# Kernel optimization log

Measured on AMD Instinct MI355X. Metric: run time of the kernel, lower is better.

Reference implementation:

```python
import jax, jax.numpy as jnp
import numpy as np
import math

BL, N, T, C, H = 16, 256, 32, 256, 4
HD = C // H
GEOM_DIM = 12
K_REL = 32
LN_EPS = 1e-5
GEPS = 1e-6
NEG = -1e9


def setup_inputs() -> dict:
    key = jax.random.key(0)
    ks = jax.random.split(key, 24)
    s = 0.02  # weight init scale
    d = {
        "x": jax.random.normal(ks[0], (BL, N, C), jnp.float32),
        "lang_fea": jax.random.normal(ks[1], (BL, T, C), jnp.float32),
        "centers": jax.random.normal(ks[2], (BL, N, 3), jnp.float32),
        "corners": jax.random.normal(ks[3], (BL, N, 8, 3), jnp.float32),
        "obj_mask": jnp.ones((BL, N), dtype=bool),
        # LayerNorm
        "ln_g": jnp.ones((C,), jnp.float32),
        "ln_b": jnp.zeros((C,), jnp.float32),
        # qkv / proj
        "W_qkv": s * jax.random.normal(ks[4], (C, 3 * C), jnp.float32),
        "b_qkv": jnp.zeros((3 * C,), jnp.float32),
        "W_proj": s * jax.random.normal(ks[5], (C, C), jnp.float32),
        "b_proj": jnp.zeros((C,), jnp.float32),
        # geom2bias MLP (12 -> C -> H)
        "Wg1": s * jax.random.normal(ks[6], (GEOM_DIM, C), jnp.float32),
        "bg1": jnp.zeros((C,), jnp.float32),
        "Wg2": s * jax.random.normal(ks[7], (C, H), jnp.float32),
        "bg2": jnp.zeros((H,), jnp.float32),
        # txt2head MLP (C -> C -> H)
        "Wt1": s * jax.random.normal(ks[8], (C, C), jnp.float32),
        "bt1": jnp.zeros((C,), jnp.float32),
        "Wt2": s * jax.random.normal(ks[9], (C, H), jnp.float32),
        "bt2": jnp.zeros((H,), jnp.float32),
        "alpha": jnp.float32(0.05),
    }
    return d


def _build_relation_geom(centers, corners):
    # centers: (BL,N,3), corners: (BL,N,8,3) -> (BL,N,N,12)
    rel_vec = centers[:, None, :, :] - centers[:, :, None, :]  # (BL,N,N,3) j - i
    dist = jnp.linalg.norm(rel_vec, axis=-1, keepdims=True)
    horiz_dist = jnp.linalg.norm(rel_vec[..., :2], axis=-1, keepdims=True)
    delta_z = rel_vec[..., 2:3]
    cos_elev = delta_z / (dist + GEPS)
    sizes = corners.max(axis=2) - corners.min(axis=2)  # (BL,N,3)
    size_i = sizes[:, :, None, :]
    size_j = sizes[:, None, :, :]
    size_diff = size_j - size_i
    size_ratio = size_j / (size_i + GEPS)
    return jnp.concatenate([rel_vec, dist, horiz_dist, cos_elev, size_diff, size_ratio], axis=-1)


def _knn_mask(centers, k):
    # (BL,N,N) bool: each row i keeps its k nearest columns j (incl. self)
    diff = centers[:, :, None, :] - centers[:, None, :, :]
    dist = jnp.linalg.norm(diff, axis=-1)  # (BL,N,N)
    _, idx = jax.lax.top_k(-dist, k)  # smallest-k indices, (BL,N,k)
    return jnp.any(jax.nn.one_hot(idx, dist.shape[-1], dtype=bool), axis=-2)


def reference(x, lang_fea, centers, corners, obj_mask, ln_g, ln_b,
              W_qkv, b_qkv, W_proj, b_proj, Wg1, bg1, Wg2, bg2,
              Wt1, bt1, Wt2, bt2, alpha):
    # geometric pairwise bias: (BL,N,N,12) -> MLP -> (BL,H,N,N)
    geom = _build_relation_geom(centers, corners)
    bias = jax.nn.gelu(geom @ Wg1 + bg1, approximate=False) @ Wg2 + bg2
    bias = jnp.transpose(bias, (0, 3, 1, 2))  # (BL,H,N,N)

    # language-conditioned head gate: (BL,H,1,1)
    sent = lang_fea.mean(axis=1)  # (BL,C)
    head_w = jax.nn.sigmoid(jax.nn.gelu(sent @ Wt1 + bt1, approximate=False) @ Wt2 + bt2)
    head_w = head_w[:, :, None, None]

    warm = 1.0  # epoch=None -> no warmup scaling

    knn_mask = _knn_mask(centers, K_REL)
    pair = obj_mask[:, :, None] & obj_mask[:, None, :]
    attn_mask = knn_mask & pair  # (BL,N,N)

    residual = x
    # LayerNorm
    mu = x.mean(axis=-1, keepdims=True)
    var = x.var(axis=-1, keepdims=True)
    xn = (x - mu) * jax.lax.rsqrt(var + LN_EPS) * ln_g + ln_b

    qkv = (xn @ W_qkv + b_qkv).reshape(BL, N, 3, H, HD)
    q = jnp.transpose(qkv[:, :, 0], (0, 2, 1, 3))  # (BL,H,N,HD)
    k = jnp.transpose(qkv[:, :, 1], (0, 2, 1, 3))
    v = jnp.transpose(qkv[:, :, 2], (0, 2, 1, 3))

    logits = jnp.einsum("bhid,bhjd->bhij", q, k) / math.sqrt(HD)
    bias_eff = warm * alpha * head_w * bias
    logits = logits + bias_eff
    logits = jnp.where(attn_mask[:, None, :, :], logits, NEG)

    attn = jax.nn.softmax(logits, axis=-1)  # dropout is identity at eval
    out = jnp.einsum("bhij,bhjd->bhid", attn, v)
    out = jnp.transpose(out, (0, 2, 1, 3)).reshape(BL, N, C)
    out = out @ W_proj + b_proj
    x_out = residual + out
    return (x_out, jax.lax.stop_gradient(attn), jax.lax.stop_gradient(bias_eff))
```

## Files before the change

### kernel.cpp

```cpp
#include <hip/hip_runtime.h>
#include <math.h>

#define BLn 16
#define Nn 256
#define Tn 32
#define Cn 256
#define Hn 4
#define HDn 64
#define KREL 32

typedef float f32x4 __attribute__((ext_vector_type(4)));
typedef __bf16 bf16x8 __attribute__((ext_vector_type(8)));
typedef _Float16 f16x4 __attribute__((ext_vector_type(4)));
typedef _Float16 f16x2 __attribute__((ext_vector_type(2)));

#define MFMA16(a, b, c) __builtin_amdgcn_mfma_f32_16x16x32_bf16(a, b, c, 0, 0, 0)
#define MFMA16H(a, b, c) __builtin_amdgcn_mfma_f32_16x16x16f16(a, b, c, 0, 0, 0)

__device__ __forceinline__ float gelu_exact(float x) {
    return 0.5f * x * (1.0f + erff(x * 0.70710678118654752440f));
}

__device__ __forceinline__ f16x2 gelu_pk(f16x2 x) {
    const f16x2 P4 = {(_Float16)4.0f, (_Float16)4.0f};
    const f16x2 M4 = {(_Float16)-4.0f, (_Float16)-4.0f};
    const f16x2 C0 = {(_Float16)0.833076f, (_Float16)0.833076f};
    const f16x2 C1 = {(_Float16)-0.139388f, (_Float16)-0.139388f};
    const f16x2 C2 = {(_Float16)0.013040f, (_Float16)0.013040f};
    const f16x2 C3 = {(_Float16)-0.000413f, (_Float16)-0.000413f};
    const f16x2 HF = {(_Float16)0.5f, (_Float16)0.5f};
    f16x2 xc = __builtin_elementwise_min(__builtin_elementwise_max(x, M4), P4);
    f16x2 v = xc * xc;
    f16x2 w = C3 * v + C2;
    w = w * v + C1;
    w = w * v + C0;
    f16x2 t = w * xc;
    f16x2 s = t * HF + HF;
    return x * s;
}

__global__ void __launch_bounds__(256) k_prep(
    const float* __restrict__ x, const float* __restrict__ ln_g, const float* __restrict__ ln_b,
    __bf16* __restrict__ xnb, const float* __restrict__ centers, const int* __restrict__ obj,
    unsigned char* __restrict__ knn, const float* __restrict__ corners,
    float* __restrict__ sizes, const float* __restrict__ lang, const float* __restrict__ Wt1,
    const float* __restrict__ bt1, const float* __restrict__ Wt2, const float* __restrict__ bt2,
    float* __restrict__ headw, const float* __restrict__ W_qkv, __bf16* __restrict__ wqT,
    const float* __restrict__ W_proj, __bf16* __restrict__ wpT) {
    __shared__ float4 d4[64];
    __shared__ float sm1[Nn];
    __shared__ float ss[4], qq[4];
    __shared__ float T[64][65];
    float* sm0 = (float*)d4;
    int blk = blockIdx.x;
    int tid = threadIdx.x;

    if (blk < 4096) {
        int row = blk;
        int c = tid;
        float v = x[(size_t)row * Cn + c];
        float s = v, q = v * v;
        for (int m = 32; m > 0; m >>= 1) {
            s += __shfl_xor(s, m, 64);
            q += __shfl_xor(q, m, 64);
        }
        int w = c >> 6, l = c & 63;
        if (l == 0) { ss[w] = s; qq[w] = q; }
        __syncthreads();
        s = ss[0] + ss[1] + ss[2] + ss[3];
        q = qq[0] + qq[1] + qq[2] + qq[3];
        float mu = s * (1.0f / Cn);
        float var = q * (1.0f / Cn) - mu * mu;
        float r = rsqrtf(var + 1e-5f);
        xnb[(size_t)row * Cn + c] = (__bf16)((v - mu) * r * ln_g[c] + ln_b[c]);
    } else if (blk < 8192) {
        int bi = blk - 4096;
        int b = bi >> 8, i = bi & 255;
        int j = tid;
        float cx = centers[(b * Nn + i) * 3 + 0];
        float cy = centers[(b * Nn + i) * 3 + 1];
        float cz = centers[(b * Nn + i) * 3 + 2];
        float dx = centers[(b * Nn + j) * 3 + 0] - cx;
        float dy = centers[(b * Nn + j) * 3 + 1] - cy;
        float dz = centers[(b * Nn + j) * 3 + 2] - cz;
        float dd = sqrtf(dx * dx + dy * dy + dz * dz);
        sm0[j] = dd;
        __syncthreads();
        int rank = 0;
        for (int t4 = 0; t4 < 64; t4++) {
            float4 o = d4[t4];
            int t = t4 * 4;
            rank += (o.x < dd) || (o.x == dd && t + 0 < j);
            rank += (o.y < dd) || (o.y == dd && t + 1 < j);
            rank += (o.z < dd) || (o.z == dd && t + 2 < j);
            rank += (o.w < dd) || (o.w == dd && t + 3 < j);
        }
        bool m = (rank < KREL);
        m = m && (obj[b * Nn + i] != 0) && (obj[b * Nn + j] != 0);
        knn[(size_t)bi * Nn + j] = m ? 1 : 0;
    } else if (blk < 8208) {
        int b = blk - 8192, n = tid;
        const float* p = corners + (size_t)((b * Nn + n) * 8) * 3;
        float mn[3] = {1e30f, 1e30f, 1e30f}, mx[3] = {-1e30f, -1e30f, -1e30f};
        for (int v = 0; v < 8; v++)
            for (int d = 0; d < 3; d++) {
                float t = p[v * 3 + d];
                mn[d] = fminf(mn[d], t);
                mx[d] = fmaxf(mx[d], t);
            }
        for (int d = 0; d < 3; d++) sizes[(b * Nn + n) * 3 + d] = mx[d] - mn[d];
    } else if (blk < 8224) {
        int b = blk - 8208, c = tid;
        float s = 0.0f;
        for (int t = 0; t < Tn; t++) s += lang[((size_t)b * Tn + t) * Cn + c];
        sm0[c] = s * (1.0f / Tn);
        __syncthreads();
        float acc = bt1[c];
        for (int i = 0; i < Cn; i++) acc += sm0[i] * Wt1[i * Cn + c];
        sm1[c] = gelu_exact(acc);
        __syncthreads();
        if (c < Hn) {
            float a = bt2[c];
            for (int i = 0; i < Cn; i++) a += sm1[i] * Wt2[i * Hn + c];
            headw[b * Hn + c] = 1.0f / (1.0f + expf(-a));
        }
    } else if (blk < 8272) {
        int t = blk - 8224;
        int kt = t & 3, ot = t >> 2;
        for (int itr = 0; itr < 16; itr++) {
            int idx = itr * 256 + tid;
            int r = idx >> 6, c = idx & 63;
            T[r][c] = W_qkv[(size_t)(kt * 64 + r) * 768 + ot * 64 + c];
        }
        __syncthreads();
        for (int itr = 0; itr < 16; itr++) {
            int idx = itr * 256 + tid;
            int r = idx >> 6, c = idx & 63;
            wqT[(size_t)(ot * 64 + r) * 256 + kt * 64 + c] = (__bf16)T[c][r];
        }
    } else {
        int t = blk - 8272;
        int kt = t & 3, ot = t >> 2;
        for (int itr = 0; itr < 16; itr++) {
            int idx = itr * 256 + tid;
            int r = idx >> 6, c = idx & 63;
            T[r][c] = W_proj[(size_t)(kt * 64 + r) * 256 + ot * 64 + c];
        }
        __syncthreads();
        for (int itr = 0; itr < 16; itr++) {
            int idx = itr * 256 + tid;
            int r = idx >> 6, c = idx & 63;
            wpT[(size_t)(ot * 64 + r) * 256 + kt * 64 + c] = (__bf16)T[c][r];
        }
    }
}

__global__ void __launch_bounds__(256, 7) k_heavy(
    const float* __restrict__ centers, const float* __restrict__ sizes,
    const float* __restrict__ Wg1, const float* __restrict__ bg1,
    const float* __restrict__ Wg2, const float* __restrict__ bg2,
    const float* __restrict__ headw, const float* __restrict__ alphap,
    float* __restrict__ bias_eff, const __bf16* __restrict__ xnb,
    const __bf16* __restrict__ wqT, const float* __restrict__ bqkv,
    __bf16* __restrict__ qkvb) {
    __shared__ __align__(16) _Float16 fT[Nn][20];
    __shared__ __align__(16) _Float16 W1T[Cn][20];
    __shared__ __align__(16) _Float16 W2T[4][264];

    int blk = blockIdx.x;
    int tid = threadIdx.x;

    if (blk >= 4096) {
        int t = blk - 4096;
        int ib = t & 63, y = t >> 6;
        int w = tid >> 6, l = tid & 63, lr = l & 15, lg = l >> 4;
        const __bf16* arow = xnb + (size_t)(ib * 64 + w * 16 + lr) * Cn;

        f32x4 acc[4];
#pragma unroll
        for (int ot = 0; ot < 4; ot++) acc[ot] = (f32x4){0.f, 0.f, 0.f, 0.f};
#pragma unroll
        for (int kc = 0; kc < 8; kc++) {
            bf16x8 af = *(const bf16x8*)(arow + kc * 32 + lg * 8);
#pragma unroll
            for (int ot = 0; ot < 4; ot++) {
                bf16x8 bfr = *(const bf16x8*)(wqT + (size_t)(y * 64 + ot * 16 + lr) * Cn +
                                              kc * 32 + lg * 8);
                acc[ot] = MFMA16(af, bfr, acc[ot]);
            }
        }
        int seg = y >> 2, h = y & 3;
        __bf16* segp = qkvb + (size_t)seg * 1048576;
#pragma unroll
        for (int ot = 0; ot < 4; ot++) {
            float bo = bqkv[y * 64 + ot * 16 + lr];
#pragma unroll
            for (int r = 0; r < 4; r++) {
                int ig = ib * 64 + w * 16 + lg * 4 + r;
                int b = ig >> 8, n = ig & 255;
                segp[(((size_t)(b * Hn + h)) * Nn + n) * HDn + ot * 16 + lr] =
                    (__bf16)(acc[ot][r] + bo);
            }
        }
        return;
    }

    int b = blk >> 8, i = blk & 255;

    {
        int c = tid;
        _Float16 t1[20];
#pragma unroll
        for (int k = 0; k < 12; k++) t1[k] = (_Float16)Wg1[k * Cn + c];
        t1[12] = (_Float16)bg1[c];
#pragma unroll
        for (int k = 13; k < 20; k++) t1[k] = (_Float16)0.f;
#pragma unroll
        for (int q = 0; q < 5; q++) *(uint2*)&W1T[c][q * 4] = *(uint2*)&t1[q * 4];
#pragma unroll
        for (int h = 0; h < Hn; h++) W2T[h][c] = (_Float16)Wg2[c * Hn + h];
    }
    {
        int j = tid;
        float ci0 = centers[(b * Nn + i) * 3 + 0];
        float ci1 = centers[(b * Nn + i) * 3 + 1];
        float ci2 = centers[(b * Nn + i) * 3 + 2];
        float si0 = sizes[(b * Nn + i) * 3 + 0];
        float si1 = sizes[(b * Nn + i) * 3 + 1];
        float si2 = sizes[(b * Nn + i) * 3 + 2];
        float cj0 = centers[(b * Nn + j) * 3 + 0];
        float cj1 = centers[(b * Nn + j) * 3 + 1];
        float cj2 = centers[(b * Nn + j) * 3 + 2];
        float sj0 = sizes[(b * Nn + j) * 3 + 0];
        float sj1 = sizes[(b * Nn + j) * 3 + 1];
        float sj2 = sizes[(b * Nn + j) * 3 + 2];
        float rx = cj0 - ci0, ry = cj1 - ci1, rz = cj2 - ci2;
        float h2 = rx * rx + ry * ry;
        float dist = sqrtf(h2 + rz * rz);
        float horiz = sqrtf(h2);
        float f[16];
        f[0] = rx; f[1] = ry; f[2] = rz;
        f[3] = dist; f[4] = horiz;
        f[5] = rz / (dist + 1e-6f);
        f[6] = sj0 - si0; f[7] = sj1 - si1; f[8] = sj2 - si2;
        f[9] = sj0 / (si0 + 1e-6f);
        f[10] = sj1 / (si1 + 1e-6f);
        f[11] = sj2 / (si2 + 1e-6f);
        f[12] = 1.0f;
        _Float16 tf[20];
#pragma unroll
        for (int k = 0; k < 13; k++) tf[k] = (_Float16)f[k];
#pragma unroll
        for (int k = 13; k < 20; k++) tf[k] = (_Float16)0.f;
#pragma unroll
        for (int q = 0; q < 5; q++) *(uint2*)&fT[j][q * 4] = *(uint2*)&tf[q * 4];
    }
    __syncthreads();

    int w = tid >> 6, l = tid & 63;
    int lr = l & 15, lg = l >> 4;
    int jw = w * 64;
    int lrc = (lr < Hn) ? lr : 3;
    bool hr = (lr < Hn);

    f32x4 zero4 = {0.f, 0.f, 0.f, 0.f};
    f16x4 zf4 = {(_Float16)0.f, (_Float16)0.f, (_Float16)0.f, (_Float16)0.f};

    f16x4 bf_[4];
#pragma unroll
    for (int jt = 0; jt < 4; jt++) bf_[jt] = *(const f16x4*)&fT[jw + jt * 16 + lr][lg * 4];

    f32x4 pacc[4];
#pragma unroll
    for (int jt = 0; jt < 4; jt++) pacc[jt] = zero4;

#pragma unroll 2
    for (int cw = 0; cw < 16; cw++) {
        int cbase = cw * 16;
        f16x4 aw = *(const f16x4*)&W1T[cbase + lr][lg * 4];
        f16x4 w2v = *(const f16x4*)&W2T[lrc][cbase + lg * 4];
        f16x4 b2 = hr ? w2v : zf4;
#pragma unroll
        for (int jt = 0; jt < 4; jt++) {
            f32x4 acc = MFMA16H(aw, bf_[jt], zero4);
            f16x2 h01 = __builtin_bit_cast(f16x2, __builtin_amdgcn_cvt_pkrtz(acc[0], acc[1]));
            f16x2 h23 = __builtin_bit_cast(f16x2, __builtin_amdgcn_cvt_pkrtz(acc[2], acc[3]));
            h01 = gelu_pk(h01);
            h23 = gelu_pk(h23);
            f16x4 ga;
            ga[0] = h01[0]; ga[1] = h01[1]; ga[2] = h23[0]; ga[3] = h23[1];
            pacc[jt] = MFMA16H(ga, b2, pacc[jt]);
        }
    }

    float alpha = alphap[0];
    if (hr) {
        float hw_ = headw[b * Hn + lr];
        float bg = bg2[lr];
        float* dst = bias_eff + (((size_t)(b * Hn + lr)) * Nn + i) * Nn;
#pragma unroll
        for (int jt = 0; jt < 4; jt++) {
            f32x4 o4;
#pragma unroll
            for (int r = 0; r < 4; r++) o4[r] = alpha * hw_ * (pacc[jt][r] + bg);
            *(f32x4*)&dst[jw + jt * 16 + lg * 4] = o4;
        }
    }
}

__global__ void __launch_bounds__(128) k_attn(const __bf16* __restrict__ qkvb,
                                              const float* __restrict__ bias_eff,
                                              const unsigned char* __restrict__ knn,
                                              float* __restrict__ attn_out,
                                              __bf16* __restrict__ houtb) {
    __shared__ __bf16 Vt[64][264];
    __shared__ __bf16 Plds[2][16][136];
    int blk = blockIdx.x;
    int bh = blk >> 3, it = blk & 7;
    int b = bh >> 2, h = bh & 3;
    int tid = threadIdx.x;

    const __bf16* vbase = qkvb + 2 * 1048576 + (size_t)bh * (Nn * HDn);
#pragma unroll
    for (int jh = 0; jh < 2; jh++) {
        int j = jh * 128 + tid;
#pragma unroll
        for (int c8 = 0; c8 < 8; c8++) {
            bf16x8 v8 = *(const bf16x8*)(vbase + (size_t)j * HDn + c8 * 8);
#pragma unroll
            for (int e = 0; e < 8; e++) Vt[c8 * 8 + e][j] = v8[e];
        }
    }
    __syncthreads();

    int w = tid >> 6, l = tid & 63;
    int lr = l & 15, lg = l >> 4;
    int i_glob = it * 32 + w * 16 + lr;

    const __bf16* qrow = qkvb + (size_t)bh * (Nn * HDn) + (size_t)i_glob * HDn;
    bf16x8 qf0 = *(const bf16x8*)(qrow + lg * 8);
    bf16x8 qf1 = *(const bf16x8*)(qrow + 32 + lg * 8);

    const __bf16* kbase = qkvb + 1048576 + (size_t)bh * (Nn * HDn);
    f32x4 s[16];
#pragma unroll
    for (int jt = 0; jt < 16; jt++) {
        const __bf16* krow = kbase + (size_t)(jt * 16 + lr) * HDn;
        bf16x8 ka = *(const bf16x8*)(krow + lg * 8);
        bf16x8 kb = *(const bf16x8*)(krow + 32 + lg * 8);
        f32x4 acc = (f32x4){0.f, 0.f, 0.f, 0.f};
        acc = MFMA16(ka, qf0, acc);
        acc = MFMA16(kb, qf1, acc);
        s[jt] = acc;
    }

    const float* brow = bias_eff + ((size_t)bh * Nn + i_glob) * Nn;
    const unsigned int* mrow = (const unsigned int*)(knn + ((size_t)(b * Nn + i_glob)) * Nn);
    float mx = -1e30f;
#pragma unroll
    for (int jt = 0; jt < 16; jt++) {
        f32x4 bi = *(const f32x4*)(brow + jt * 16 + lg * 4);
        unsigned int mk = mrow[jt * 4 + lg];
#pragma unroll
        for (int r = 0; r < 4; r++) {
            float v = fmaf(s[jt][r], 0.125f, bi[r]);
            v = ((mk >> (8 * r)) & 0xff) ? v : -1e9f;
            s[jt][r] = v;
            mx = fmaxf(mx, v);
        }
    }
    mx = fmaxf(mx, __shfl_xor(mx, 16, 64));
    mx = fmaxf(mx, __shfl_xor(mx, 32, 64));
    float sum = 0.0f;
#pragma unroll
    for (int jt = 0; jt < 16; jt++)
#pragma unroll
        for (int r = 0; r < 4; r++) {
            float e = __builtin_amdgcn_exp2f((s[jt][r] - mx) * 1.44269504f);
            s[jt][r] = e;
            sum += e;
        }
    sum += __shfl_xor(sum, 16, 64);
    sum += __shfl_xor(sum, 32, 64);
    float inv = 1.0f / sum;

    float* arow = attn_out + ((size_t)bh * Nn + i_glob) * Nn;
#pragma unroll
    for (int jt = 0; jt < 16; jt++) {
        f32x4 o4;
#pragma unroll
        for (int r = 0; r < 4; r++) {
            float a = s[jt][r] * inv;
            s[jt][r] = a;
            o4[r] = a;
        }
        *(f32x4*)(arow + jt * 16 + lg * 4) = o4;
    }

    f32x4 o[4];
#pragma unroll
    for (int dt = 0; dt < 4; dt++) o[dt] = (f32x4){0.f, 0.f, 0.f, 0.f};
    for (int half = 0; half < 2; half++) {
#pragma unroll
        for (int jr = 0; jr < 8; jr++) {
            int jt = half * 8 + jr;
            __bf16 pb[4];
#pragma unroll
            for (int r = 0; r < 4; r++) pb[r] = (__bf16)s[jt][r];
            *(uint2*)&Plds[w][lr][jr * 16 + lg * 4] = *(uint2*)pb;
        }
#pragma unroll
        for (int kk = 0; kk < 4; kk++) {
            bf16x8 pfrag = *(const bf16x8*)&Plds[w][lr][kk * 32 + lg * 8];
#pragma unroll
            for (int dt = 0; dt < 4; dt++) {
                bf16x8 vfrag = *(const bf16x8*)&Vt[dt * 16 + lr][half * 128 + kk * 32 + lg * 8];
                o[dt] = MFMA16(vfrag, pfrag, o[dt]);
            }
        }
    }

    __bf16* hrow = houtb + ((size_t)(b * Nn + i_glob)) * Cn + h * HDn;
#pragma unroll
    for (int dt = 0; dt < 4; dt++) {
        __bf16 hb[4];
#pragma unroll
        for (int r = 0; r < 4; r++) hb[r] = (__bf16)o[dt][r];
        *(uint2*)(hrow + dt * 16 + lg * 4) = *(uint2*)hb;
    }
}

__global__ void __launch_bounds__(256) k_proj(const __bf16* __restrict__ houtb,
                                              const __bf16* __restrict__ wpT,
                                              const float* __restrict__ bp,
                                              const float* __restrict__ x,
                                              float* __restrict__ xout) {
    int ib = blockIdx.x, y = blockIdx.y;
    int tid = threadIdx.x;
    int w = tid >> 6, l = tid & 63, lr = l & 15, lg = l >> 4;
    const __bf16* arow = houtb + (size_t)(ib * 64 + w * 16 + lr) * Cn;

    f32x4 acc[4];
#pragma unroll
    for (int ot = 0; ot < 4; ot++) acc[ot] = (f32x4){0.f, 0.f, 0.f, 0.f};
#pragma unroll
    for (int kc = 0; kc < 8; kc++) {
        bf16x8 af = *(const bf16x8*)(arow + kc * 32 + lg * 8);
#pragma unroll
        for (int ot = 0; ot < 4; ot++) {
            bf16x8 bfr = *(const bf16x8*)(wpT + (size_t)(y * 64 + ot * 16 + lr) * Cn +
                                          kc * 32 + lg * 8);
            acc[ot] = MFMA16(af, bfr, acc[ot]);
        }
    }
#pragma unroll
    for (int ot = 0; ot < 4; ot++) {
        int o = y * 64 + ot * 16 + lr;
        float bo = bp[o];
#pragma unroll
        for (int r = 0; r < 4; r++) {
            int ig = ib * 64 + w * 16 + lg * 4 + r;
            size_t idx = (size_t)ig * Cn + o;
            xout[idx] = x[idx] + bo + acc[ot][r];
        }
    }
}

extern "C" void kernel_launch(void* const* d_in, const int* in_sizes, int n_in,
                              void* d_out, int out_size, void* d_ws, size_t ws_size,
                              hipStream_t stream) {
    const float* x       = (const float*)d_in[0];
    const float* lang    = (const float*)d_in[1];
    const float* centers = (const float*)d_in[2];
    const float* corners = (const float*)d_in[3];
    const int*   obj     = (const int*)d_in[4];
    const float* ln_g    = (const float*)d_in[5];
    const float* ln_b    = (const float*)d_in[6];
    const float* W_qkv   = (const float*)d_in[7];
    const float* b_qkv   = (const float*)d_in[8];
    const float* W_proj  = (const float*)d_in[9];
    const float* b_proj  = (const float*)d_in[10];
    const float* Wg1     = (const float*)d_in[11];
    const float* bg1     = (const float*)d_in[12];
    const float* Wg2     = (const float*)d_in[13];
    const float* bg2     = (const float*)d_in[14];
    const float* Wt1     = (const float*)d_in[15];
    const float* bt1     = (const float*)d_in[16];
    const float* Wt2     = (const float*)d_in[17];
    const float* bt2     = (const float*)d_in[18];
    const float* alpha   = (const float*)d_in[19];

    float* out = (float*)d_out;
    float* xout     = out;
    float* attn     = out + 1048576;
    float* bias_eff = out + 5242880;

    __bf16* xnb   = (__bf16*)d_ws;
    __bf16* qkvb  = xnb + 1048576;
    __bf16* houtb = qkvb + 3145728;
    __bf16* wqT   = houtb + 1048576;
    __bf16* wpT   = wqT + 196608;
    float*  sizes = (float*)(wpT + 65536);
    float*  headw = sizes + 12288;
    unsigned char* knn = (unsigned char*)(headw + 64);

    k_prep<<<8288, 256, 0, stream>>>(x, ln_g, ln_b, xnb, centers, obj, knn, corners, sizes,
                                     lang, Wt1, bt1, Wt2, bt2, headw, W_qkv, wqT, W_proj, wpT);
    k_heavy<<<4864, 256, 0, stream>>>(centers, sizes, Wg1, bg1, Wg2, bg2, headw, alpha,
                                      bias_eff, xnb, wqT, b_qkv, qkvb);
    k_attn<<<512, 128, 0, stream>>>(qkvb, bias_eff, knn, attn, houtb);
    k_proj<<<dim3(64, 4), 256, 0, stream>>>(houtb, wpT, b_proj, x, xout);
}
```

Before: 123.2 us.

## Store V pre-transposed from QKV GEMM and drop LDS transpose in attention

The QKV projection epilogue now writes V in a transposed (d-major) layout, so the attention kernel reads V fragments straight from global memory. This removes the per-block LDS transpose of V and its barrier, and the 33KB shared buffer, which should allow more attention blocks per CU. The geometry MLP loop is also restructured to issue all four first-layer MFMAs before the GELU and second-layer MFMAs, and k_heavy's launch bound hint drops from 7 to 4 waves to relax register pressure. The risk is that V is now reread from global or L2 by every block instead of once into LDS.

```diff
diff --git a/kernel.cpp b/kernel.cpp
--- a/kernel.cpp
+++ b/kernel.cpp
@@ -155,7 +155,7 @@
     }
 }
 
-__global__ void __launch_bounds__(256, 7) k_heavy(
+__global__ void __launch_bounds__(256, 4) k_heavy(
     const float* __restrict__ centers, const float* __restrict__ sizes,
     const float* __restrict__ Wg1, const float* __restrict__ bg1,
     const float* __restrict__ Wg2, const float* __restrict__ bg2,
@@ -190,16 +190,31 @@
             }
         }
         int seg = y >> 2, h = y & 3;
-        __bf16* segp = qkvb + (size_t)seg * 1048576;
-#pragma unroll
-        for (int ot = 0; ot < 4; ot++) {
-            float bo = bqkv[y * 64 + ot * 16 + lr];
-#pragma unroll
-            for (int r = 0; r < 4; r++) {
-                int ig = ib * 64 + w * 16 + lg * 4 + r;
-                int b = ig >> 8, n = ig & 255;
-                segp[(((size_t)(b * Hn + h)) * Nn + n) * HDn + ot * 16 + lr] =
-                    (__bf16)(acc[ot][r] + bo);
+        int b = (ib * 64) >> 8;
+        if (seg < 2) {
+            __bf16* segp = qkvb + (size_t)seg * 1048576;
+#pragma unroll
+            for (int ot = 0; ot < 4; ot++) {
+                float bo = bqkv[y * 64 + ot * 16 + lr];
+#pragma unroll
+                for (int r = 0; r < 4; r++) {
+                    int ig = ib * 64 + w * 16 + lg * 4 + r;
+                    int n = ig & 255;
+                    segp[(((size_t)(b * Hn + h)) * Nn + n) * HDn + ot * 16 + lr] =
+                        (__bf16)(acc[ot][r] + bo);
+                }
+            }
+        } else {
+            __bf16* vT = qkvb + 2 * 1048576 + (size_t)(b * Hn + h) * (HDn * Nn);
+            int n0 = (ib * 64 + w * 16 + lg * 4) & 255;
+#pragma unroll
+            for (int ot = 0; ot < 4; ot++) {
+                int d = ot * 16 + lr;
+                float bo = bqkv[y * 64 + d];
+                __bf16 pb[4];
+#pragma unroll
+                for (int r = 0; r < 4; r++) pb[r] = (__bf16)(acc[ot][r] + bo);
+                *(uint2*)(vT + (size_t)d * Nn + n0) = *(uint2*)pb;
             }
         }
         return;
@@ -280,17 +295,23 @@
         f16x4 aw = *(const f16x4*)&W1T[cbase + lr][lg * 4];
         f16x4 w2v = *(const f16x4*)&W2T[lrc][cbase + lg * 4];
         f16x4 b2 = hr ? w2v : zf4;
+        f32x4 acc[4];
+#pragma unroll
+        for (int jt = 0; jt < 4; jt++) acc[jt] = MFMA16H(aw, bf_[jt], zero4);
+        f16x4 ga[4];
 #pragma unroll
         for (int jt = 0; jt < 4; jt++) {
-            f32x4 acc = MFMA16H(aw, bf_[jt], zero4);
-            f16x2 h01 = __builtin_bit_cast(f16x2, __builtin_amdgcn_cvt_pkrtz(acc[0], acc[1]));
-            f16x2 h23 = __builtin_bit_cast(f16x2, __builtin_amdgcn_cvt_pkrtz(acc[2], acc[3]));
+            f16x2 h01 =
+                __builtin_bit_cast(f16x2, __builtin_amdgcn_cvt_pkrtz(acc[jt][0], acc[jt][1]));
+            f16x2 h23 =
+                __builtin_bit_cast(f16x2, __builtin_amdgcn_cvt_pkrtz(acc[jt][2], acc[jt][3]));
             h01 = gelu_pk(h01);
             h23 = gelu_pk(h23);
-            f16x4 ga;
-            ga[0] = h01[0]; ga[1] = h01[1]; ga[2] = h23[0]; ga[3] = h23[1];
-            pacc[jt] = MFMA16H(ga, b2, pacc[jt]);
-        }
+            ga[jt][0] = h01[0]; ga[jt][1] = h01[1];
+            ga[jt][2] = h23[0]; ga[jt][3] = h23[1];
+        }
+#pragma unroll
+        for (int jt = 0; jt < 4; jt++) pacc[jt] = MFMA16H(ga[jt], b2, pacc[jt]);
     }
 
     float alpha = alphap[0];
@@ -313,25 +334,11 @@
                                               const unsigned char* __restrict__ knn,
                                               float* __restrict__ attn_out,
                                               __bf16* __restrict__ houtb) {
-    __shared__ __bf16 Vt[64][264];
     __shared__ __bf16 Plds[2][16][136];
     int blk = blockIdx.x;
     int bh = blk >> 3, it = blk & 7;
     int b = bh >> 2, h = bh & 3;
     int tid = threadIdx.x;
-
-    const __bf16* vbase = qkvb + 2 * 1048576 + (size_t)bh * (Nn * HDn);
-#pragma unroll
-    for (int jh = 0; jh < 2; jh++) {
-        int j = jh * 128 + tid;
-#pragma unroll
-        for (int c8 = 0; c8 < 8; c8++) {
-            bf16x8 v8 = *(const bf16x8*)(vbase + (size_t)j * HDn + c8 * 8);
-#pragma unroll
-            for (int e = 0; e < 8; e++) Vt[c8 * 8 + e][j] = v8[e];
-        }
-    }
-    __syncthreads();
 
     int w = tid >> 6, l = tid & 63;
     int lr = l & 15, lg = l >> 4;
@@ -397,6 +404,7 @@
         *(f32x4*)(arow + jt * 16 + lg * 4) = o4;
     }
 
+    const __bf16* vT = qkvb + 2 * 1048576 + (size_t)bh * (HDn * Nn);
     f32x4 o[4];
 #pragma unroll
     for (int dt = 0; dt < 4; dt++) o[dt] = (f32x4){0.f, 0.f, 0.f, 0.f};
@@ -414,7 +422,8 @@
             bf16x8 pfrag = *(const bf16x8*)&Plds[w][lr][kk * 32 + lg * 8];
 #pragma unroll
             for (int dt = 0; dt < 4; dt++) {
-                bf16x8 vfrag = *(const bf16x8*)&Vt[dt * 16 + lr][half * 128 + kk * 32 + lg * 8];
+                bf16x8 vfrag = *(const bf16x8*)(vT + (size_t)(dt * 16 + lr) * Nn + half * 128 +
+                                                kk * 32 + lg * 8);
                 o[dt] = MFMA16(vfrag, pfrag, o[dt]);
             }
         }
```

New measurement: 133.2 us. 8.1% more time.
